# Kernel tuning notes

Hardware: AMD Instinct MI355X
Metric: run time of the kernel (lower is better)

Reference implementation:

```python
import jax, jax.numpy as jnp
import numpy as np

E_DIM = 1024
HID = 4096
H = (2 * HID) // 3  # floor(2*hidden/3) = 2730
NUM_EXPERTS = 8
TOP_K = 2
LN_EPS = 1e-5


def setup_inputs() -> dict:
    key = jax.random.key(0)
    ks = jax.random.split(key, 10)
    B, T, P = 2, 8, 256
    s_in = 1.0 / np.sqrt(E_DIM)
    s_h = 1.0 / np.sqrt(H)
    return {
        "x": jax.random.normal(ks[0], (B, T, P, E_DIM), jnp.float32),
        "Wr": jax.random.normal(ks[1], (NUM_EXPERTS, E_DIM), jnp.float32) * s_in,
        "Wv": jax.random.normal(ks[2], (NUM_EXPERTS, E_DIM, H), jnp.float32) * s_in,
        "bv": jax.random.normal(ks[3], (NUM_EXPERTS, H), jnp.float32) * 0.01,
        "Wg": jax.random.normal(ks[4], (NUM_EXPERTS, E_DIM, H), jnp.float32) * s_in,
        "bg": jax.random.normal(ks[5], (NUM_EXPERTS, H), jnp.float32) * 0.01,
        "Wo": jax.random.normal(ks[6], (NUM_EXPERTS, H, E_DIM), jnp.float32) * s_h,
        "bo": jax.random.normal(ks[7], (NUM_EXPERTS, E_DIM), jnp.float32) * 0.01,
        "ln_g": jnp.ones((E_DIM,), jnp.float32),
        "ln_b": jnp.zeros((E_DIM,), jnp.float32),
    }


def reference(x, Wr, Wv, bv, Wg, bg, Wo, bo, ln_g, ln_b):
    B, T, P, E = x.shape
    flat = x.reshape(-1, E)          # [N, E]
    N = flat.shape[0]

    # router: top-k logits -> softmax combine weights
    logits = flat @ Wr.T                              # [N, C]
    tk_vals, tk_idx = jax.lax.top_k(logits, TOP_K)    # [N, K]
    tk_w = jax.nn.softmax(tk_vals, axis=-1)           # [N, K]

    # dense combine-weight matrix: zero for non-routed experts
    comb = jnp.zeros((N, NUM_EXPERTS), flat.dtype)
    comb = comb.at[jnp.arange(N)[:, None], tk_idx].add(tk_w)  # [N, C]

    # all experts over all tokens (masked combine makes this exact)
    hv = jnp.einsum('ne,ceh->cnh', flat, Wv) + bv[:, None, :]  # [C, N, H]
    hg = jnp.einsum('ne,ceh->cnh', flat, Wg) + bg[:, None, :]
    h = jax.nn.silu(hv) * hg                                   # SwiGLU
    oe = jnp.einsum('cnh,che->cne', h, Wo) + bo[:, None, :]    # [C, N, E]
    out = jnp.einsum('cne,nc->ne', oe, comb)                   # weighted combine

    # residual + LayerNorm (AdaptiveNormalizer with no conditioning)
    y = x + out.reshape(B, T, P, E)
    mu = jnp.mean(y, axis=-1, keepdims=True)
    var = jnp.mean((y - mu) ** 2, axis=-1, keepdims=True)
    return ln_g * (y - mu) * jax.lax.rsqrt(var + LN_EPS) + ln_b
```

## Files before the change

kernel.cpp:

```cpp
#include <hip/hip_runtime.h>
#include <hip/hip_bf16.h>

#define E_DIM 1024
#define HDIM  2730
#define HP    2752
#define NEXP  8
#define NTOK  4096
#define NPAIR 8192
#define NSLOT 72
#define LN_EPS 1e-5f

typedef __attribute__((ext_vector_type(8))) short  short8;
typedef __attribute__((ext_vector_type(4))) short  short4v;
typedef __attribute__((ext_vector_type(4))) float  floatx4;
typedef __attribute__((ext_vector_type(4))) int    intx4;

__device__ __forceinline__ __hip_bfloat16 f2bf(float f) { return __float2bfloat16(f); }

__global__ __launch_bounds__(256) void router_k(const float* __restrict__ x,
    const float* __restrict__ Wr, int* __restrict__ counts,
    int* __restrict__ tk_idx, float* __restrict__ tk_w) {
  int wid = threadIdx.x >> 6, lane = threadIdx.x & 63;
  int t = blockIdx.x * 4 + wid;
  const float* xr = x + (size_t)t * E_DIM;
  float xv[16];
#pragma unroll
  for (int i = 0; i < 16; ++i) xv[i] = xr[lane + 64 * i];
  float lg[8];
#pragma unroll
  for (int e = 0; e < 8; ++e) {
    const float* wr = Wr + e * E_DIM;
    float a = 0.f;
#pragma unroll
    for (int i = 0; i < 16; ++i) a += xv[i] * wr[lane + 64 * i];
#pragma unroll
    for (int o = 32; o; o >>= 1) a += __shfl_xor(a, o, 64);
    lg[e] = a;
  }
  if (lane == 0) {
    int i0 = 0; float l0 = lg[0];
#pragma unroll
    for (int e = 1; e < 8; ++e) if (lg[e] > l0) { l0 = lg[e]; i0 = e; }
    int i1 = -1; float l1 = -1e30f;
#pragma unroll
    for (int e = 0; e < 8; ++e) if (e != i0 && lg[e] > l1) { l1 = lg[e]; i1 = e; }
    float w0 = 1.f / (1.f + __expf(l1 - l0));
    atomicAdd(&counts[i0], 1);
    atomicAdd(&counts[i1], 1);
    tk_idx[2 * t]     = i0;  tk_idx[2 * t + 1] = i1;
    tk_w[2 * t]       = w0;  tk_w[2 * t + 1]   = 1.f - w0;
  }
}

__global__ void offsets_k(const int* __restrict__ counts, int* __restrict__ offsets,
                          int* __restrict__ cursor,
                          int* __restrict__ slot_e, int* __restrict__ slot_m0) {
  if (threadIdx.x == 0) {
    int off = 0, s = 0;
    for (int e = 0; e < NEXP; ++e) {
      offsets[e] = off; cursor[e] = off;
      for (int m0 = 0; m0 < counts[e]; m0 += 128) { slot_e[s] = e; slot_m0[s] = m0; ++s; }
      off += counts[e];
    }
    for (; s < NSLOT; ++s) { slot_e[s] = -1; slot_m0[s] = 0; }
  }
}

__global__ __launch_bounds__(256) void scatter_k(const int* __restrict__ tk_idx,
    const float* __restrict__ tk_w, int* __restrict__ cursor,
    int* __restrict__ pair_token, float* __restrict__ pair_w, int* __restrict__ pair_pos) {
  int t = blockIdx.x * 256 + threadIdx.x;
#pragma unroll
  for (int k = 0; k < 2; ++k) {
    int e = tk_idx[2 * t + k];
    int pos = atomicAdd(&cursor[e], 1);
    pair_token[pos] = t;
    pair_w[pos] = tk_w[2 * t + k];
    pair_pos[2 * t + k] = pos;
  }
}

__global__ __launch_bounds__(256) void gatherx_k(const float* __restrict__ x,
    const int* __restrict__ pair_token, __hip_bfloat16* __restrict__ xs) {
  int p = blockIdx.x;
  int t = pair_token[p];
  const float* src = x + (size_t)t * E_DIM;
  __hip_bfloat16* dst = xs + (size_t)p * E_DIM;
  int i = threadIdx.x * 4;
  floatx4 v = *(const floatx4*)(src + i);
  union { __hip_bfloat16 h[4]; short4v s; } u;
#pragma unroll
  for (int j = 0; j < 4; ++j) u.h[j] = f2bf(v[j]);
  *(short4v*)(dst + i) = u.s;
}

__global__ __launch_bounds__(256) void tcvt_k(const float* __restrict__ in,
    __hip_bfloat16* __restrict__ out, int R, int C, int outRS,
    size_t inExpStride, size_t outExpStride) {
  __shared__ float tile[64 * 65];
  int e = blockIdx.z;
  const float* ip = in + inExpStride * e;
  __hip_bfloat16* op = out + outExpStride * e;
  int c0 = blockIdx.x * 64, r0 = blockIdx.y * 64;
#pragma unroll
  for (int i = 0; i < 16; ++i) {
    int idx = i * 256 + threadIdx.x;
    int rr = idx >> 6, cc = idx & 63;
    int gr = r0 + rr, gc = c0 + cc;
    tile[rr * 65 + cc] = (gr < R && gc < C) ? ip[(size_t)gr * C + gc] : 0.f;
  }
  __syncthreads();
#pragma unroll
  for (int i = 0; i < 2; ++i) {
    int idx = i * 256 + threadIdx.x;
    int cc = idx >> 3, rb = (idx & 7) * 8;
    union { __hip_bfloat16 h[8]; intx4 v; } u;
#pragma unroll
    for (int j = 0; j < 8; ++j) u.h[j] = f2bf(tile[(rb + j) * 65 + cc]);
    *(intx4*)(op + (size_t)(c0 + cc) * outRS + (r0 + rb)) = u.v;
  }
}

__global__ __launch_bounds__(256) void gemm1_k(
    const __hip_bfloat16* __restrict__ xs,
    const int* __restrict__ counts, const int* __restrict__ offsets,
    const int* __restrict__ slot_e, const int* __restrict__ slot_m0,
    const float* __restrict__ bv, const float* __restrict__ bg,
    const __hip_bfloat16* __restrict__ WvT, const __hip_bfloat16* __restrict__ WgT,
    __hip_bfloat16* __restrict__ h) {
  int slot = blockIdx.y;
  int e = slot_e[slot];
  if (e < 0) return;
  int m0 = slot_m0[slot];
  int Me = counts[e], off = offsets[e];
  int n0 = blockIdx.x * 64;

  __shared__ __hip_bfloat16 sA[2 * 128 * 40];
  __shared__ __hip_bfloat16 sBv[2 * 64 * 40];
  __shared__ __hip_bfloat16 sBg[2 * 64 * 40];

  int tid = threadIdx.x;
  int wid = tid >> 6, lane = tid & 63;
  int wm = wid >> 1, wn = wid & 1;
  int q = lane >> 4, r = lane & 15;

  int srow = tid >> 3;
  int kk   = (tid & 7) * 8;
  int ks   = kk >> 5, k2 = kk & 31;
  const __hip_bfloat16* gA  = xs + (size_t)(off + m0 + srow) * E_DIM + kk;
  size_t bb = (size_t)e * ((size_t)HP * E_DIM) + (size_t)(n0 + srow) * E_DIM + kk;
  const __hip_bfloat16* gBv = WvT + bb;
  const __hip_bfloat16* gBg = WgT + bb;
  __hip_bfloat16* wA  = sA  + ks * (128 * 40) + srow * 40 + k2;
  __hip_bfloat16* wBv = sBv + ks * (64 * 40) + srow * 40 + k2;
  __hip_bfloat16* wBg = sBg + ks * (64 * 40) + srow * 40 + k2;

  floatx4 accv[4][2], accg[4][2];
  floatx4 zz = {0.f, 0.f, 0.f, 0.f};
#pragma unroll
  for (int mi = 0; mi < 4; ++mi)
#pragma unroll
    for (int ni = 0; ni < 2; ++ni) { accv[mi][ni] = zz; accg[mi][ni] = zz; }

  for (int kt = 0; kt < E_DIM / 64; ++kt) {
    size_t ko = (size_t)kt * 64;
#pragma unroll
    for (int i = 0; i < 4; ++i)
      *(intx4*)(wA + i * 32 * 40) = *(const intx4*)(gA + ko + (size_t)i * 32 * E_DIM);
#pragma unroll
    for (int i = 0; i < 2; ++i) {
      *(intx4*)(wBv + i * 32 * 40) = *(const intx4*)(gBv + ko + (size_t)i * 32 * E_DIM);
      *(intx4*)(wBg + i * 32 * 40) = *(const intx4*)(gBg + ko + (size_t)i * 32 * E_DIM);
    }
    __syncthreads();
#pragma unroll
    for (int s = 0; s < 2; ++s) {
      const __hip_bfloat16* pA  = sA  + s * (128 * 40);
      const __hip_bfloat16* pBv = sBv + s * (64 * 40);
      const __hip_bfloat16* pBg = sBg + s * (64 * 40);
      short8 av[4];
#pragma unroll
      for (int mi = 0; mi < 4; ++mi)
        av[mi] = *(const short8*)(pA + (wm * 64 + mi * 16 + r) * 40 + q * 8);
#pragma unroll
      for (int ni = 0; ni < 2; ++ni) {
        short8 b8v = *(const short8*)(pBv + (wn * 32 + ni * 16 + r) * 40 + q * 8);
        short8 b8g = *(const short8*)(pBg + (wn * 32 + ni * 16 + r) * 40 + q * 8);
#pragma unroll
        for (int mi = 0; mi < 4; ++mi) {
          accv[mi][ni] = __builtin_amdgcn_mfma_f32_16x16x32_bf16(av[mi], b8v, accv[mi][ni], 0, 0, 0);
          accg[mi][ni] = __builtin_amdgcn_mfma_f32_16x16x32_bf16(av[mi], b8g, accg[mi][ni], 0, 0, 0);
        }
      }
    }
    __syncthreads();
  }

#pragma unroll
  for (int mi = 0; mi < 4; ++mi) {
#pragma unroll
    for (int rr = 0; rr < 4; ++rr) {
      int m_loc = wm * 64 + mi * 16 + q * 4 + rr;
      int m = m0 + m_loc;
      if (m >= Me) continue;
      size_t hrow = (size_t)(off + m) * HP;
#pragma unroll
      for (int ni = 0; ni < 2; ++ni) {
        int n = n0 + wn * 32 + ni * 16 + r;
        float bvv = (n < HDIM) ? bv[e * HDIM + n] : 0.f;
        float bgv = (n < HDIM) ? bg[e * HDIM + n] : 0.f;
        float hv = accv[mi][ni][rr] + bvv;
        float hg = accg[mi][ni][rr] + bgv;
        float sgm = 1.f / (1.f + __expf(-hv));
        h[hrow + n] = f2bf(hv * sgm * hg);
      }
    }
  }
}

__global__ __launch_bounds__(256) void gemm2_k(
    const __hip_bfloat16* __restrict__ hb,
    const int* __restrict__ counts, const int* __restrict__ offsets,
    const int* __restrict__ slot_e, const int* __restrict__ slot_m0,
    const float* __restrict__ bo,
    const __hip_bfloat16* __restrict__ WoT,
    float* __restrict__ pout) {
  int slot = blockIdx.y;
  int e = slot_e[slot];
  if (e < 0) return;
  int m0 = slot_m0[slot];
  int Me = counts[e], off = offsets[e];
  int n0 = blockIdx.x * 64;

  __shared__ __hip_bfloat16 sA[2 * 128 * 40];
  __shared__ __hip_bfloat16 sB[2 * 64 * 40];

  int tid = threadIdx.x;
  int wid = tid >> 6, lane = tid & 63;
  int wm = wid >> 1, wn = wid & 1;
  int q = lane >> 4, r = lane & 15;

  int srow = tid >> 3;
  int kk   = (tid & 7) * 8;
  int ks   = kk >> 5, k2 = kk & 31;
  const __hip_bfloat16* gA = hb + (size_t)(off + m0 + srow) * HP + kk;
  const __hip_bfloat16* gB =
      WoT + (size_t)e * ((size_t)E_DIM * HP) + (size_t)(n0 + srow) * HP + kk;
  __hip_bfloat16* wA = sA + ks * (128 * 40) + srow * 40 + k2;
  __hip_bfloat16* wB = sB + ks * (64 * 40) + srow * 40 + k2;

  floatx4 acc[4][2];
  floatx4 zz = {0.f, 0.f, 0.f, 0.f};
#pragma unroll
  for (int mi = 0; mi < 4; ++mi)
#pragma unroll
    for (int ni = 0; ni < 2; ++ni) acc[mi][ni] = zz;

  for (int kt = 0; kt < HP / 64; ++kt) {
    size_t ko = (size_t)kt * 64;
#pragma unroll
    for (int i = 0; i < 4; ++i)
      *(intx4*)(wA + i * 32 * 40) = *(const intx4*)(gA + ko + (size_t)i * 32 * HP);
#pragma unroll
    for (int i = 0; i < 2; ++i)
      *(intx4*)(wB + i * 32 * 40) = *(const intx4*)(gB + ko + (size_t)i * 32 * HP);
    __syncthreads();
#pragma unroll
    for (int s = 0; s < 2; ++s) {
      const __hip_bfloat16* pA = sA + s * (128 * 40);
      const __hip_bfloat16* pB = sB + s * (64 * 40);
      short8 av[4];
#pragma unroll
      for (int mi = 0; mi < 4; ++mi)
        av[mi] = *(const short8*)(pA + (wm * 64 + mi * 16 + r) * 40 + q * 8);
#pragma unroll
      for (int ni = 0; ni < 2; ++ni) {
        short8 b8 = *(const short8*)(pB + (wn * 32 + ni * 16 + r) * 40 + q * 8);
#pragma unroll
        for (int mi = 0; mi < 4; ++mi)
          acc[mi][ni] = __builtin_amdgcn_mfma_f32_16x16x32_bf16(av[mi], b8, acc[mi][ni], 0, 0, 0);
      }
    }
    __syncthreads();
  }

#pragma unroll
  for (int mi = 0; mi < 4; ++mi) {
#pragma unroll
    for (int rr = 0; rr < 4; ++rr) {
      int m_loc = wm * 64 + mi * 16 + q * 4 + rr;
      int m = m0 + m_loc;
      if (m >= Me) continue;
      size_t orow = (size_t)(off + m) * E_DIM;
#pragma unroll
      for (int ni = 0; ni < 2; ++ni) {
        int n = n0 + wn * 32 + ni * 16 + r;
        pout[orow + n] = acc[mi][ni][rr] + bo[e * E_DIM + n];
      }
    }
  }
}

__global__ __launch_bounds__(256) void ln_k(const float* __restrict__ x,
    const float* __restrict__ pout, const int* __restrict__ pair_pos,
    const float* __restrict__ pair_w, const float* __restrict__ ln_g,
    const float* __restrict__ ln_b, float* __restrict__ out) {
  int t = blockIdx.x, tid = threadIdx.x;
  int p0 = pair_pos[2 * t], p1 = pair_pos[2 * t + 1];
  float w0 = pair_w[p0], w1 = pair_w[p1];
  const float* xr = x + (size_t)t * E_DIM;
  const float* r0 = pout + (size_t)p0 * E_DIM;
  const float* r1 = pout + (size_t)p1 * E_DIM;
  float y[4];
  float s = 0.f, ss = 0.f;
#pragma unroll
  for (int i = 0; i < 4; ++i) {
    int e = tid + 256 * i;
    y[i] = xr[e] + w0 * r0[e] + w1 * r1[e];
    s += y[i];
    ss += y[i] * y[i];
  }
#pragma unroll
  for (int o = 32; o; o >>= 1) { s += __shfl_xor(s, o, 64); ss += __shfl_xor(ss, o, 64); }
  __shared__ float red[8];
  int wid = tid >> 6, lane = tid & 63;
  if (lane == 0) { red[wid] = s; red[4 + wid] = ss; }
  __syncthreads();
  s  = red[0] + red[1] + red[2] + red[3];
  ss = red[4] + red[5] + red[6] + red[7];
  float mu = s * (1.f / E_DIM);
  float var = ss * (1.f / E_DIM) - mu * mu;
  float rs = rsqrtf(var + LN_EPS);
#pragma unroll
  for (int i = 0; i < 4; ++i) {
    int e = tid + 256 * i;
    out[(size_t)t * E_DIM + e] = ln_g[e] * (y[i] - mu) * rs + ln_b[e];
  }
}

extern "C" void kernel_launch(void* const* d_in, const int* in_sizes, int n_in,
                              void* d_out, int out_size, void* d_ws, size_t ws_size,
                              hipStream_t stream) {
  const float* x    = (const float*)d_in[0];
  const float* Wr   = (const float*)d_in[1];
  const float* Wv   = (const float*)d_in[2];
  const float* bv   = (const float*)d_in[3];
  const float* Wg   = (const float*)d_in[4];
  const float* bg   = (const float*)d_in[5];
  const float* Wo   = (const float*)d_in[6];
  const float* bo   = (const float*)d_in[7];
  const float* ln_g = (const float*)d_in[8];
  const float* ln_b = (const float*)d_in[9];
  float* out = (float*)d_out;

  char* ws = (char*)d_ws;
  size_t off = 0;
  auto alloc = [&](size_t bytes) -> void* {
    void* p = ws + off;
    off = (off + bytes + 255) & ~(size_t)255;
    return p;
  };
  int*   counts     = (int*)alloc(32);
  int*   cursor     = (int*)alloc(32);
  int*   offsets    = (int*)alloc(32);
  int*   slot_e     = (int*)alloc(NSLOT * 4);
  int*   slot_m0    = (int*)alloc(NSLOT * 4);
  int*   tk_idx     = (int*)alloc((size_t)NTOK * 2 * 4);
  float* tk_w       = (float*)alloc((size_t)NTOK * 2 * 4);
  int*   pair_token = (int*)alloc((size_t)NPAIR * 4);
  float* pair_w     = (float*)alloc((size_t)NPAIR * 4);
  int*   pair_pos   = (int*)alloc((size_t)NPAIR * 4);
  __hip_bfloat16* xs   = (__hip_bfloat16*)alloc((size_t)(NPAIR + 128) * E_DIM * 2);
  __hip_bfloat16* hbuf = (__hip_bfloat16*)alloc((size_t)(NPAIR + 128) * HP * 2);
  float* pout = (float*)alloc((size_t)NPAIR * E_DIM * 4);

  size_t welems = (size_t)NEXP * HP * E_DIM;
  __hip_bfloat16* WvT = (__hip_bfloat16*)alloc(welems * 2);
  __hip_bfloat16* WgT = (__hip_bfloat16*)alloc(welems * 2);
  __hip_bfloat16* WoT = (__hip_bfloat16*)alloc(welems * 2);

  hipMemsetAsync(d_ws, 0, 1024, stream);

  router_k<<<NTOK / 4, 256, 0, stream>>>(x, Wr, counts, tk_idx, tk_w);
  offsets_k<<<1, 64, 0, stream>>>(counts, offsets, cursor, slot_e, slot_m0);
  scatter_k<<<NTOK / 256, 256, 0, stream>>>(tk_idx, tk_w, cursor, pair_token, pair_w, pair_pos);
  gatherx_k<<<NPAIR, 256, 0, stream>>>(x, pair_token, xs);

  tcvt_k<<<dim3(HP / 64, E_DIM / 64, NEXP), 256, 0, stream>>>(
      Wv, WvT, E_DIM, HDIM, E_DIM, (size_t)E_DIM * HDIM, (size_t)HP * E_DIM);
  tcvt_k<<<dim3(HP / 64, E_DIM / 64, NEXP), 256, 0, stream>>>(
      Wg, WgT, E_DIM, HDIM, E_DIM, (size_t)E_DIM * HDIM, (size_t)HP * E_DIM);
  tcvt_k<<<dim3(E_DIM / 64, HP / 64, NEXP), 256, 0, stream>>>(
      Wo, WoT, HDIM, E_DIM, HP, (size_t)HDIM * E_DIM, (size_t)E_DIM * HP);

  gemm1_k<<<dim3(HP / 64, NSLOT), 256, 0, stream>>>(
      xs, counts, offsets, slot_e, slot_m0, bv, bg, WvT, WgT, hbuf);
  gemm2_k<<<dim3(E_DIM / 64, NSLOT), 256, 0, stream>>>(
      hbuf, counts, offsets, slot_e, slot_m0, bo, WoT, pout);

  ln_k<<<NTOK, 256, 0, stream>>>(x, pout, pair_pos, pair_w, ln_g, ln_b, out);
}
```

Measured before the change: 733.2 us.

## Use 32x32 MFMA with 128x128 tiles and register prefetch in expert GEMMs

Both expert GEMMs move from 128x64 tiles built on 16x16x32 MFMA to 128x128 tiles built on 32x32x16 MFMA. The next K-slice is prefetched into registers while the current one is computed, and launch bounds now request two blocks per CU. The aim is more reuse of each loaded tile, fewer LDS reads per FLOP and less exposed global-load latency. In exchange, Wv/Wg are padded to 2816 rows, which adds padded compute and convert work, and the xs and pout buffers now share workspace memory; the offsets kernel also fills its slot table in parallel.

```diff
diff --git a/kernel.cpp b/kernel.cpp
--- a/kernel.cpp
+++ b/kernel.cpp
@@ -4,16 +4,18 @@
 #define E_DIM 1024
 #define HDIM  2730
 #define HP    2752
+#define HP2   2816
 #define NEXP  8
 #define NTOK  4096
 #define NPAIR 8192
 #define NSLOT 72
 #define LN_EPS 1e-5f
 
-typedef __attribute__((ext_vector_type(8))) short  short8;
-typedef __attribute__((ext_vector_type(4))) short  short4v;
-typedef __attribute__((ext_vector_type(4))) float  floatx4;
-typedef __attribute__((ext_vector_type(4))) int    intx4;
+typedef __attribute__((ext_vector_type(8)))  short short8;
+typedef __attribute__((ext_vector_type(4)))  short short4v;
+typedef __attribute__((ext_vector_type(4)))  float floatx4;
+typedef __attribute__((ext_vector_type(16))) float floatx16;
+typedef __attribute__((ext_vector_type(4)))  int   intx4;
 
 __device__ __forceinline__ __hip_bfloat16 f2bf(float f) { return __float2bfloat16(f); }
 
@@ -55,14 +57,25 @@
 __global__ void offsets_k(const int* __restrict__ counts, int* __restrict__ offsets,
                           int* __restrict__ cursor,
                           int* __restrict__ slot_e, int* __restrict__ slot_m0) {
-  if (threadIdx.x == 0) {
-    int off = 0, s = 0;
+  __shared__ int cnt[NEXP], tbase[NEXP + 1];
+  int tid = threadIdx.x;
+  if (tid == 0) {
+    int off = 0, tb = 0;
     for (int e = 0; e < NEXP; ++e) {
-      offsets[e] = off; cursor[e] = off;
-      for (int m0 = 0; m0 < counts[e]; m0 += 128) { slot_e[s] = e; slot_m0[s] = m0; ++s; }
-      off += counts[e];
-    }
-    for (; s < NSLOT; ++s) { slot_e[s] = -1; slot_m0[s] = 0; }
+      int c = counts[e];
+      cnt[e] = c;
+      offsets[e] = off; cursor[e] = off; off += c;
+      tbase[e] = tb; tb += (c + 127) >> 7;
+    }
+    tbase[NEXP] = tb;
+  }
+  __syncthreads();
+  if (tid < NEXP) {
+    int nt = (cnt[tid] + 127) >> 7, b = tbase[tid];
+    for (int i = 0; i < nt; ++i) { slot_e[b + i] = tid; slot_m0[b + i] = i * 128; }
+  }
+  for (int s = tbase[NEXP] + tid; s < NSLOT; s += blockDim.x) {
+    slot_e[s] = -1; slot_m0[s] = 0;
   }
 }
 
@@ -121,7 +134,7 @@
   }
 }
 
-__global__ __launch_bounds__(256) void gemm1_k(
+__global__ __launch_bounds__(256, 2) void gemm1_k(
     const __hip_bfloat16* __restrict__ xs,
     const int* __restrict__ counts, const int* __restrict__ offsets,
     const int* __restrict__ slot_e, const int* __restrict__ slot_m0,
@@ -133,92 +146,94 @@
   if (e < 0) return;
   int m0 = slot_m0[slot];
   int Me = counts[e], off = offsets[e];
-  int n0 = blockIdx.x * 64;
-
-  __shared__ __hip_bfloat16 sA[2 * 128 * 40];
-  __shared__ __hip_bfloat16 sBv[2 * 64 * 40];
-  __shared__ __hip_bfloat16 sBg[2 * 64 * 40];
+  int n0 = blockIdx.x * 128;
+
+  __shared__ __hip_bfloat16 sA[128 * 40];
+  __shared__ __hip_bfloat16 sBv[128 * 40];
+  __shared__ __hip_bfloat16 sBg[128 * 40];
 
   int tid = threadIdx.x;
   int wid = tid >> 6, lane = tid & 63;
   int wm = wid >> 1, wn = wid & 1;
-  int q = lane >> 4, r = lane & 15;
-
-  int srow = tid >> 3;
-  int kk   = (tid & 7) * 8;
-  int ks   = kk >> 5, k2 = kk & 31;
-  const __hip_bfloat16* gA  = xs + (size_t)(off + m0 + srow) * E_DIM + kk;
-  size_t bb = (size_t)e * ((size_t)HP * E_DIM) + (size_t)(n0 + srow) * E_DIM + kk;
+  int l31 = lane & 31, q = lane >> 5;
+
+  int srow = tid >> 2, sc = (tid & 3) * 8;
+  const __hip_bfloat16* gA = xs + (size_t)(off + m0 + srow) * E_DIM + sc;
+  size_t bb = (size_t)e * ((size_t)HP2 * E_DIM) + (size_t)(n0 + srow) * E_DIM + sc;
   const __hip_bfloat16* gBv = WvT + bb;
   const __hip_bfloat16* gBg = WgT + bb;
-  __hip_bfloat16* wA  = sA  + ks * (128 * 40) + srow * 40 + k2;
-  __hip_bfloat16* wBv = sBv + ks * (64 * 40) + srow * 40 + k2;
-  __hip_bfloat16* wBg = sBg + ks * (64 * 40) + srow * 40 + k2;
-
-  floatx4 accv[4][2], accg[4][2];
-  floatx4 zz = {0.f, 0.f, 0.f, 0.f};
-#pragma unroll
-  for (int mi = 0; mi < 4; ++mi)
-#pragma unroll
-    for (int ni = 0; ni < 2; ++ni) { accv[mi][ni] = zz; accg[mi][ni] = zz; }
-
-  for (int kt = 0; kt < E_DIM / 64; ++kt) {
-    size_t ko = (size_t)kt * 64;
-#pragma unroll
-    for (int i = 0; i < 4; ++i)
-      *(intx4*)(wA + i * 32 * 40) = *(const intx4*)(gA + ko + (size_t)i * 32 * E_DIM);
-#pragma unroll
-    for (int i = 0; i < 2; ++i) {
-      *(intx4*)(wBv + i * 32 * 40) = *(const intx4*)(gBv + ko + (size_t)i * 32 * E_DIM);
-      *(intx4*)(wBg + i * 32 * 40) = *(const intx4*)(gBg + ko + (size_t)i * 32 * E_DIM);
-    }
+  const size_t rstep = (size_t)64 * E_DIM;
+
+  floatx16 accv[2][2], accg[2][2];
+#pragma unroll
+  for (int mi = 0; mi < 2; ++mi)
+#pragma unroll
+    for (int ni = 0; ni < 2; ++ni) {
+      accv[mi][ni] = (floatx16)(0.f);
+      accg[mi][ni] = (floatx16)(0.f);
+    }
+
+  intx4 rA0, rA1, rV0, rV1, rG0, rG1;
+  rA0 = *(const intx4*)(gA);          rA1 = *(const intx4*)(gA + rstep);
+  rV0 = *(const intx4*)(gBv);         rV1 = *(const intx4*)(gBv + rstep);
+  rG0 = *(const intx4*)(gBg);         rG1 = *(const intx4*)(gBg + rstep);
+
+  const int NK = E_DIM / 32;
+  for (int kt = 0; kt < NK; ++kt) {
+    *(intx4*)(sA  + srow * 40 + sc) = rA0;  *(intx4*)(sA  + (srow + 64) * 40 + sc) = rA1;
+    *(intx4*)(sBv + srow * 40 + sc) = rV0;  *(intx4*)(sBv + (srow + 64) * 40 + sc) = rV1;
+    *(intx4*)(sBg + srow * 40 + sc) = rG0;  *(intx4*)(sBg + (srow + 64) * 40 + sc) = rG1;
     __syncthreads();
+    if (kt + 1 < NK) {
+      int k0 = (kt + 1) * 32;
+      rA0 = *(const intx4*)(gA + k0);  rA1 = *(const intx4*)(gA + k0 + rstep);
+      rV0 = *(const intx4*)(gBv + k0); rV1 = *(const intx4*)(gBv + k0 + rstep);
+      rG0 = *(const intx4*)(gBg + k0); rG1 = *(const intx4*)(gBg + k0 + rstep);
+    }
 #pragma unroll
     for (int s = 0; s < 2; ++s) {
-      const __hip_bfloat16* pA  = sA  + s * (128 * 40);
-      const __hip_bfloat16* pBv = sBv + s * (64 * 40);
-      const __hip_bfloat16* pBg = sBg + s * (64 * 40);
-      short8 av[4];
-#pragma unroll
-      for (int mi = 0; mi < 4; ++mi)
-        av[mi] = *(const short8*)(pA + (wm * 64 + mi * 16 + r) * 40 + q * 8);
-#pragma unroll
-      for (int ni = 0; ni < 2; ++ni) {
-        short8 b8v = *(const short8*)(pBv + (wn * 32 + ni * 16 + r) * 40 + q * 8);
-        short8 b8g = *(const short8*)(pBg + (wn * 32 + ni * 16 + r) * 40 + q * 8);
-#pragma unroll
-        for (int mi = 0; mi < 4; ++mi) {
-          accv[mi][ni] = __builtin_amdgcn_mfma_f32_16x16x32_bf16(av[mi], b8v, accv[mi][ni], 0, 0, 0);
-          accg[mi][ni] = __builtin_amdgcn_mfma_f32_16x16x32_bf16(av[mi], b8g, accg[mi][ni], 0, 0, 0);
-        }
+      int ko = s * 16 + q * 8;
+      short8 a0 = *(const short8*)(sA + (wm * 64 + l31) * 40 + ko);
+      short8 a1 = *(const short8*)(sA + (wm * 64 + 32 + l31) * 40 + ko);
+      short8 v0 = *(const short8*)(sBv + (wn * 64 + l31) * 40 + ko);
+      short8 v1 = *(const short8*)(sBv + (wn * 64 + 32 + l31) * 40 + ko);
+      short8 g0 = *(const short8*)(sBg + (wn * 64 + l31) * 40 + ko);
+      short8 g1 = *(const short8*)(sBg + (wn * 64 + 32 + l31) * 40 + ko);
+      accv[0][0] = __builtin_amdgcn_mfma_f32_32x32x16_bf16(a0, v0, accv[0][0], 0, 0, 0);
+      accv[0][1] = __builtin_amdgcn_mfma_f32_32x32x16_bf16(a0, v1, accv[0][1], 0, 0, 0);
+      accv[1][0] = __builtin_amdgcn_mfma_f32_32x32x16_bf16(a1, v0, accv[1][0], 0, 0, 0);
+      accv[1][1] = __builtin_amdgcn_mfma_f32_32x32x16_bf16(a1, v1, accv[1][1], 0, 0, 0);
+      accg[0][0] = __builtin_amdgcn_mfma_f32_32x32x16_bf16(a0, g0, accg[0][0], 0, 0, 0);
+      accg[0][1] = __builtin_amdgcn_mfma_f32_32x32x16_bf16(a0, g1, accg[0][1], 0, 0, 0);
+      accg[1][0] = __builtin_amdgcn_mfma_f32_32x32x16_bf16(a1, g0, accg[1][0], 0, 0, 0);
+      accg[1][1] = __builtin_amdgcn_mfma_f32_32x32x16_bf16(a1, g1, accg[1][1], 0, 0, 0);
+    }
+    __syncthreads();
+  }
+
+#pragma unroll
+  for (int ni = 0; ni < 2; ++ni) {
+    int n = n0 + wn * 64 + ni * 32 + l31;
+    float bvv = (n < HDIM) ? bv[e * HDIM + n] : 0.f;
+    float bgv = (n < HDIM) ? bg[e * HDIM + n] : 0.f;
+    bool nok = (n < HP);
+#pragma unroll
+    for (int mi = 0; mi < 2; ++mi) {
+#pragma unroll
+      for (int reg = 0; reg < 16; ++reg) {
+        int row = (reg & 3) + 8 * (reg >> 2) + 4 * q;
+        int m = m0 + wm * 64 + mi * 32 + row;
+        if (m >= Me || !nok) continue;
+        float hv = accv[mi][ni][reg] + bvv;
+        float hg = accg[mi][ni][reg] + bgv;
+        float sgm = 1.f / (1.f + __expf(-hv));
+        h[(size_t)(off + m) * HP + n] = f2bf(hv * sgm * hg);
       }
     }
-    __syncthreads();
-  }
-
-#pragma unroll
-  for (int mi = 0; mi < 4; ++mi) {
-#pragma unroll
-    for (int rr = 0; rr < 4; ++rr) {
-      int m_loc = wm * 64 + mi * 16 + q * 4 + rr;
-      int m = m0 + m_loc;
-      if (m >= Me) continue;
-      size_t hrow = (size_t)(off + m) * HP;
-#pragma unroll
-      for (int ni = 0; ni < 2; ++ni) {
-        int n = n0 + wn * 32 + ni * 16 + r;
-        float bvv = (n < HDIM) ? bv[e * HDIM + n] : 0.f;
-        float bgv = (n < HDIM) ? bg[e * HDIM + n] : 0.f;
-        float hv = accv[mi][ni][rr] + bvv;
-        float hg = accg[mi][ni][rr] + bgv;
-        float sgm = 1.f / (1.f + __expf(-hv));
-        h[hrow + n] = f2bf(hv * sgm * hg);
-      }
-    }
-  }
-}
-
-__global__ __launch_bounds__(256) void gemm2_k(
+  }
+}
+
+__global__ __launch_bounds__(256, 2) void gemm2_k(
     const __hip_bfloat16* __restrict__ hb,
     const int* __restrict__ counts, const int* __restrict__ offsets,
     const int* __restrict__ slot_e, const int* __restrict__ slot_m0,
@@ -230,72 +245,78 @@
   if (e < 0) return;
   int m0 = slot_m0[slot];
   int Me = counts[e], off = offsets[e];
-  int n0 = blockIdx.x * 64;
-
-  __shared__ __hip_bfloat16 sA[2 * 128 * 40];
-  __shared__ __hip_bfloat16 sB[2 * 64 * 40];
+  int n0 = blockIdx.x * 128;
+
+  __shared__ __hip_bfloat16 sA[128 * 72];
+  __shared__ __hip_bfloat16 sB[128 * 72];
 
   int tid = threadIdx.x;
   int wid = tid >> 6, lane = tid & 63;
   int wm = wid >> 1, wn = wid & 1;
-  int q = lane >> 4, r = lane & 15;
-
-  int srow = tid >> 3;
-  int kk   = (tid & 7) * 8;
-  int ks   = kk >> 5, k2 = kk & 31;
-  const __hip_bfloat16* gA = hb + (size_t)(off + m0 + srow) * HP + kk;
+  int l31 = lane & 31, q = lane >> 5;
+
+  int srow = tid >> 3, sc = (tid & 7) * 8;
+  const __hip_bfloat16* gA = hb + (size_t)(off + m0 + srow) * HP + sc;
   const __hip_bfloat16* gB =
-      WoT + (size_t)e * ((size_t)E_DIM * HP) + (size_t)(n0 + srow) * HP + kk;
-  __hip_bfloat16* wA = sA + ks * (128 * 40) + srow * 40 + k2;
-  __hip_bfloat16* wB = sB + ks * (64 * 40) + srow * 40 + k2;
-
-  floatx4 acc[4][2];
-  floatx4 zz = {0.f, 0.f, 0.f, 0.f};
-#pragma unroll
-  for (int mi = 0; mi < 4; ++mi)
-#pragma unroll
-    for (int ni = 0; ni < 2; ++ni) acc[mi][ni] = zz;
-
-  for (int kt = 0; kt < HP / 64; ++kt) {
-    size_t ko = (size_t)kt * 64;
-#pragma unroll
-    for (int i = 0; i < 4; ++i)
-      *(intx4*)(wA + i * 32 * 40) = *(const intx4*)(gA + ko + (size_t)i * 32 * HP);
-#pragma unroll
-    for (int i = 0; i < 2; ++i)
-      *(intx4*)(wB + i * 32 * 40) = *(const intx4*)(gB + ko + (size_t)i * 32 * HP);
+      WoT + (size_t)e * ((size_t)E_DIM * HP) + (size_t)(n0 + srow) * HP + sc;
+  const size_t rstep = (size_t)32 * HP;
+
+  floatx16 acc[2][2];
+#pragma unroll
+  for (int mi = 0; mi < 2; ++mi)
+#pragma unroll
+    for (int ni = 0; ni < 2; ++ni) acc[mi][ni] = (floatx16)(0.f);
+
+  intx4 rA[4], rB[4];
+#pragma unroll
+  for (int i = 0; i < 4; ++i) {
+    rA[i] = *(const intx4*)(gA + (size_t)i * rstep);
+    rB[i] = *(const intx4*)(gB + (size_t)i * rstep);
+  }
+
+  const int NK = HP / 64;
+  for (int kt = 0; kt < NK; ++kt) {
+#pragma unroll
+    for (int i = 0; i < 4; ++i) {
+      *(intx4*)(sA + (srow + i * 32) * 72 + sc) = rA[i];
+      *(intx4*)(sB + (srow + i * 32) * 72 + sc) = rB[i];
+    }
     __syncthreads();
-#pragma unroll
-    for (int s = 0; s < 2; ++s) {
-      const __hip_bfloat16* pA = sA + s * (128 * 40);
-      const __hip_bfloat16* pB = sB + s * (64 * 40);
-      short8 av[4];
-#pragma unroll
-      for (int mi = 0; mi < 4; ++mi)
-        av[mi] = *(const short8*)(pA + (wm * 64 + mi * 16 + r) * 40 + q * 8);
-#pragma unroll
-      for (int ni = 0; ni < 2; ++ni) {
-        short8 b8 = *(const short8*)(pB + (wn * 32 + ni * 16 + r) * 40 + q * 8);
-#pragma unroll
-        for (int mi = 0; mi < 4; ++mi)
-          acc[mi][ni] = __builtin_amdgcn_mfma_f32_16x16x32_bf16(av[mi], b8, acc[mi][ni], 0, 0, 0);
+    if (kt + 1 < NK) {
+      int k0 = (kt + 1) * 64;
+#pragma unroll
+      for (int i = 0; i < 4; ++i) {
+        rA[i] = *(const intx4*)(gA + k0 + (size_t)i * rstep);
+        rB[i] = *(const intx4*)(gB + k0 + (size_t)i * rstep);
       }
     }
+#pragma unroll
+    for (int s = 0; s < 4; ++s) {
+      int ko = s * 16 + q * 8;
+      short8 a0 = *(const short8*)(sA + (wm * 64 + l31) * 72 + ko);
+      short8 a1 = *(const short8*)(sA + (wm * 64 + 32 + l31) * 72 + ko);
+      short8 b0 = *(const short8*)(sB + (wn * 64 + l31) * 72 + ko);
+      short8 b1 = *(const short8*)(sB + (wn * 64 + 32 + l31) * 72 + ko);
+      acc[0][0] = __builtin_amdgcn_mfma_f32_32x32x16_bf16(a0, b0, acc[0][0], 0, 0, 0);
+      acc[0][1] = __builtin_amdgcn_mfma_f32_32x32x16_bf16(a0, b1, acc[0][1], 0, 0, 0);
+      acc[1][0] = __builtin_amdgcn_mfma_f32_32x32x16_bf16(a1, b0, acc[1][0], 0, 0, 0);
+      acc[1][1] = __builtin_amdgcn_mfma_f32_32x32x16_bf16(a1, b1, acc[1][1], 0, 0, 0);
+    }
     __syncthreads();
   }
 
 #pragma unroll
-  for (int mi = 0; mi < 4; ++mi) {
-#pragma unroll
-    for (int rr = 0; rr < 4; ++rr) {
-      int m_loc = wm * 64 + mi * 16 + q * 4 + rr;
-      int m = m0 + m_loc;
-      if (m >= Me) continue;
-      size_t orow = (size_t)(off + m) * E_DIM;
-#pragma unroll
-      for (int ni = 0; ni < 2; ++ni) {
-        int n = n0 + wn * 32 + ni * 16 + r;
-        pout[orow + n] = acc[mi][ni][rr] + bo[e * E_DIM + n];
+  for (int ni = 0; ni < 2; ++ni) {
+    int n = n0 + wn * 64 + ni * 32 + l31;
+    float bb = bo[e * E_DIM + n];
+#pragma unroll
+    for (int mi = 0; mi < 2; ++mi) {
+#pragma unroll
+      for (int reg = 0; reg < 16; ++reg) {
+        int row = (reg & 3) + 8 * (reg >> 2) + 4 * q;
+        int m = m0 + wm * 64 + mi * 32 + row;
+        if (m >= Me) continue;
+        pout[(size_t)(off + m) * E_DIM + n] = acc[mi][ni][reg] + bb;
       }
     }
   }
@@ -370,14 +391,16 @@
   int*   pair_token = (int*)alloc((size_t)NPAIR * 4);
   float* pair_w     = (float*)alloc((size_t)NPAIR * 4);
   int*   pair_pos   = (int*)alloc((size_t)NPAIR * 4);
-  __hip_bfloat16* xs   = (__hip_bfloat16*)alloc((size_t)(NPAIR + 128) * E_DIM * 2);
+  size_t xs_bytes   = (size_t)(NPAIR + 128) * E_DIM * 2;
+  size_t pout_bytes = (size_t)NPAIR * E_DIM * 4;
+  char*  xs_pout    = (char*)alloc(xs_bytes > pout_bytes ? xs_bytes : pout_bytes);
+  __hip_bfloat16* xs = (__hip_bfloat16*)xs_pout;
+  float* pout        = (float*)xs_pout;
   __hip_bfloat16* hbuf = (__hip_bfloat16*)alloc((size_t)(NPAIR + 128) * HP * 2);
-  float* pout = (float*)alloc((size_t)NPAIR * E_DIM * 4);
-
-  size_t welems = (size_t)NEXP * HP * E_DIM;
-  __hip_bfloat16* WvT = (__hip_bfloat16*)alloc(welems * 2);
-  __hip_bfloat16* WgT = (__hip_bfloat16*)alloc(welems * 2);
-  __hip_bfloat16* WoT = (__hip_bfloat16*)alloc(welems * 2);
+
+  __hip_bfloat16* WvT = (__hip_bfloat16*)alloc((size_t)NEXP * HP2 * E_DIM * 2);
+  __hip_bfloat16* WgT = (__hip_bfloat16*)alloc((size_t)NEXP * HP2 * E_DIM * 2);
+  __hip_bfloat16* WoT = (__hip_bfloat16*)alloc((size_t)NEXP * E_DIM * HP * 2);
 
   hipMemsetAsync(d_ws, 0, 1024, stream);
 
@@ -386,16 +409,16 @@
   scatter_k<<<NTOK / 256, 256, 0, stream>>>(tk_idx, tk_w, cursor, pair_token, pair_w, pair_pos);
   gatherx_k<<<NPAIR, 256, 0, stream>>>(x, pair_token, xs);
 
-  tcvt_k<<<dim3(HP / 64, E_DIM / 64, NEXP), 256, 0, stream>>>(
-      Wv, WvT, E_DIM, HDIM, E_DIM, (size_t)E_DIM * HDIM, (size_t)HP * E_DIM);
-  tcvt_k<<<dim3(HP / 64, E_DIM / 64, NEXP), 256, 0, stream>>>(
-      Wg, WgT, E_DIM, HDIM, E_DIM, (size_t)E_DIM * HDIM, (size_t)HP * E_DIM);
+  tcvt_k<<<dim3(HP2 / 64, E_DIM / 64, NEXP), 256, 0, stream>>>(
+      Wv, WvT, E_DIM, HDIM, E_DIM, (size_t)E_DIM * HDIM, (size_t)HP2 * E_DIM);
+  tcvt_k<<<dim3(HP2 / 64, E_DIM / 64, NEXP), 256, 0, stream>>>(
+      Wg, WgT, E_DIM, HDIM, E_DIM, (size_t)E_DIM * HDIM, (size_t)HP2 * E_DIM);
   tcvt_k<<<dim3(E_DIM / 64, HP / 64, NEXP), 256, 0, stream>>>(
       Wo, WoT, HDIM, E_DIM, HP, (size_t)HDIM * E_DIM, (size_t)E_DIM * HP);
 
-  gemm1_k<<<dim3(HP / 64, NSLOT), 256, 0, stream>>>(
+  gemm1_k<<<dim3(HP2 / 128, NSLOT), 256, 0, stream>>>(
       xs, counts, offsets, slot_e, slot_m0, bv, bg, WvT, WgT, hbuf);
-  gemm2_k<<<dim3(E_DIM / 64, NSLOT), 256, 0, stream>>>(
+  gemm2_k<<<dim3(E_DIM / 128, NSLOT), 256, 0, stream>>>(
       hbuf, counts, offsets, slot_e, slot_m0, bo, WoT, pout);
 
   ln_k<<<NTOK, 256, 0, stream>>>(x, pout, pair_pos, pair_w, ln_g, ln_b, out);
```

After: 738.9 us. Within noise of the previous version (+0.8%).
